# Performance work log

Hardware: AMD Instinct MI355X
Metric: run time of the kernel (lower is better)

## Reference

```python
import jax, jax.numpy as jnp
import numpy as np

EPS = 1e-08
TEMPERATURE = 0.05


def setup_inputs() -> dict:
    key = jax.random.key(0)
    k1, k2 = jax.random.split(key)
    N = 8192
    predict_similarity = jax.random.normal(k1, (N,), dtype=jnp.float32)
    true_similarity = jax.random.uniform(k2, (N,), dtype=jnp.float32)
    return {"predict_similarity": predict_similarity, "true_similarity": true_similarity}


def reference(predict_similarity, true_similarity):
    # Sort descending by ground-truth score
    order = jnp.argsort(-true_similarity)
    yt = true_similarity[order]                      # (N,)
    yp = (predict_similarity / TEMPERATURE)[order]   # (N,)
    N = yt.shape[0]

    # Pairwise ground-truth gaps W[k, j] = yt[k] - yt[j]
    W = yt[:, None] - yt[None, :]                    # (N, N)
    # negatives: strictly later in the sorted order AND strictly lower score
    tri = jnp.triu(jnp.ones((N, N), dtype=bool), 1)
    mask = tri & (W > EPS)
    row_valid = jnp.any(mask, axis=1)                # rows contributing to the loss

    neg_inf = jnp.float32(-jnp.inf)
    # weight for the positive = max gap among its valid negatives
    weight_k = jnp.max(jnp.where(mask, W, neg_inf), axis=1)
    weight_k = jnp.where(row_valid, weight_k, 0.0)

    logit_pos = yp * weight_k                        # (N,)
    L_neg = yp[None, :] * W                          # (N, N) negative logits

    # stable masked logsumexp over {pos} U {masked negatives}
    m = jnp.maximum(logit_pos, jnp.max(jnp.where(mask, L_neg, neg_inf), axis=1))
    m = jnp.where(row_valid, m, 0.0)
    z = jnp.where(mask, L_neg - m[:, None], neg_inf)  # exp(-inf)=0 for masked-out
    sum_exp = jnp.exp(logit_pos - m) + jnp.sum(jnp.exp(z), axis=1)
    log_prob = logit_pos - m - jnp.log(sum_exp)      # log_softmax(...)[0]

    count = jnp.sum(row_valid)
    total = jnp.sum(jnp.where(row_valid, log_prob, 0.0))
    return jnp.where(count > 0, -total / jnp.maximum(count, 1).astype(total.dtype), 0.0)
```

## Files before the change

kernel.cpp:

```cpp
#include <hip/hip_runtime.h>
#include <hip/hip_bf16.h>

#define NN 8192
#define EPSF 1e-8f
#define LOG2E 1.4426950408889634f
#define LN2f 0.6931471805599453f
#define BLOCK 256
#define ROWS 4
#define ROWS_PER_BLOCK (ROWS * (BLOCK / 64))
#define RG (NN / ROWS_PER_BLOCK)
#define CHUNKS 4
#define CH (NN / CHUNKS)

#define A2SCALE (20.0f * LOG2E)

__global__ __launch_bounds__(BLOCK) void pro_main(const float* __restrict__ yt_g,
                                                  const float* __restrict__ pred_g,
                                                  float2* __restrict__ partial) {
    __shared__ float4 yt_s[CH / 4];
    __shared__ float4 a2_s[CH / 4];

    const int t = threadIdx.x;
    const int rg = blockIdx.x >> 2;
    const int c  = blockIdx.x & 3;

    const float4* ytg4 = (const float4*)(yt_g + c * CH);
    const float4* pdg4 = (const float4*)(pred_g + c * CH);
    for (int i = t; i < CH / 4; i += BLOCK) {
        yt_s[i] = ytg4[i];
        float4 p = pdg4[i];
        p.x *= A2SCALE; p.y *= A2SCALE; p.z *= A2SCALE; p.w *= A2SCALE;
        a2_s[i] = p;
    }
    __syncthreads();

    const int wave = t >> 6, lane = t & 63;
    const int row0 = rg * ROWS_PER_BLOCK + wave * ROWS;

    float x[ROWS], M[ROWS];
#pragma unroll
    for (int r = 0; r < ROWS; ++r) {
        x[r] = yt_g[row0 + r];
        M[r] = -INFINITY;
    }

    for (int i = 0; i < CH / 256; ++i) {
        float4 y4 = yt_s[i * 64 + lane];
        float4 a4 = a2_s[i * 64 + lane];
#pragma unroll
        for (int r = 0; r < ROWS; ++r) {
            float W0 = x[r] - y4.x; float L0 = a4.x * W0; M[r] = fmaxf(M[r], (W0 > EPSF) ? L0 : -INFINITY);
            float W1 = x[r] - y4.y; float L1 = a4.y * W1; M[r] = fmaxf(M[r], (W1 > EPSF) ? L1 : -INFINITY);
            float W2 = x[r] - y4.z; float L2 = a4.z * W2; M[r] = fmaxf(M[r], (W2 > EPSF) ? L2 : -INFINITY);
            float W3 = x[r] - y4.w; float L3 = a4.w * W3; M[r] = fmaxf(M[r], (W3 > EPSF) ? L3 : -INFINITY);
        }
    }
#pragma unroll
    for (int r = 0; r < ROWS; ++r) {
#pragma unroll
        for (int m = 1; m < 64; m <<= 1) M[r] = fmaxf(M[r], __shfl_xor(M[r], m));
    }

    float s[ROWS] = {0.f, 0.f, 0.f, 0.f};
    for (int i = 0; i < CH / 256; ++i) {
        float4 y4 = yt_s[i * 64 + lane];
        float4 a4 = a2_s[i * 64 + lane];
#pragma unroll
        for (int r = 0; r < ROWS; ++r) {
            float W0 = x[r] - y4.x; float t0 = __builtin_fmaf(a4.x, W0, -M[r]); s[r] += exp2f((W0 > EPSF) ? t0 : -INFINITY);
            float W1 = x[r] - y4.y; float t1 = __builtin_fmaf(a4.y, W1, -M[r]); s[r] += exp2f((W1 > EPSF) ? t1 : -INFINITY);
            float W2 = x[r] - y4.z; float t2 = __builtin_fmaf(a4.z, W2, -M[r]); s[r] += exp2f((W2 > EPSF) ? t2 : -INFINITY);
            float W3 = x[r] - y4.w; float t3 = __builtin_fmaf(a4.w, W3, -M[r]); s[r] += exp2f((W3 > EPSF) ? t3 : -INFINITY);
        }
    }
#pragma unroll
    for (int r = 0; r < ROWS; ++r) {
#pragma unroll
        for (int m = 1; m < 64; m <<= 1) s[r] += __shfl_xor(s[r], m);
    }

    if (lane == 0) {
#pragma unroll
        for (int r = 0; r < ROWS; ++r) partial[c * NN + row0 + r] = make_float2(M[r], s[r]);
    }
}

__global__ __launch_bounds__(1024) void finalize(const float* __restrict__ yt,
                                                 const float* __restrict__ pred,
                                                 const float2* __restrict__ partial,
                                                 float* __restrict__ out) {
    __shared__ float redm[16];
    __shared__ float2 red2[16];
    __shared__ float bmin;
    const int t = threadIdx.x, lane = t & 63, wave = t >> 6;

    float mn = INFINITY;
    for (int i = t; i < NN; i += 1024) mn = fminf(mn, yt[i]);
#pragma unroll
    for (int m = 1; m < 64; m <<= 1) mn = fminf(mn, __shfl_xor(mn, m));
    if (lane == 0) redm[wave] = mn;
    __syncthreads();
    if (t == 0) {
        float v = redm[0];
        for (int i = 1; i < 16; ++i) v = fminf(v, redm[i]);
        bmin = v;
    }
    __syncthreads();
    const float yt_min = bmin;

    float wtot = 0.f, wcnt = 0.f;
    for (int row = t; row < NN; row += 1024) {
        float x = yt[row];
        float w = x - yt_min;
        float a2 = pred[row] * A2SCALE;
        float lp = a2 * w;
        float2 pc[CHUNKS];
        float M = lp;
#pragma unroll
        for (int c = 0; c < CHUNKS; ++c) {
            pc[c] = partial[c * NN + row];
            M = fmaxf(M, pc[c].x);
        }
        float sum = exp2f(lp - M);
#pragma unroll
        for (int c = 0; c < CHUNKS; ++c) sum += pc[c].y * exp2f(pc[c].x - M);
        float logp = (lp - M) * LN2f - __logf(sum);
        if (w > EPSF) { wtot += logp; wcnt += 1.f; }
    }
#pragma unroll
    for (int m = 1; m < 64; m <<= 1) { wtot += __shfl_xor(wtot, m); wcnt += __shfl_xor(wcnt, m); }
    if (lane == 0) red2[wave] = make_float2(wtot, wcnt);
    __syncthreads();
    if (t == 0) {
        float bt = 0.f, bc = 0.f;
        for (int i = 0; i < 16; ++i) { bt += red2[i].x; bc += red2[i].y; }
        out[0] = (bc > 0.f) ? (-bt / bc) : 0.f;
    }
}

extern "C" void kernel_launch(void* const* d_in, const int* in_sizes, int n_in,
                              void* d_out, int out_size, void* d_ws, size_t ws_size,
                              hipStream_t stream) {
    const float* pred = (const float*)d_in[0];
    const float* yt   = (const float*)d_in[1];

    float2* partial = (float2*)d_ws;

    pro_main<<<RG * CHUNKS, BLOCK, 0, stream>>>(yt, pred, partial);
    finalize<<<1, 1024, 0, stream>>>(yt, pred, partial, (float*)d_out);
}
```

Measured before the change: 93.02 us.

## Bucket-sort scores to skip non-negative column ranges in pairwise logsumexp

Adds a single-block counting sort that buckets ground-truth scores into 8192 bins and writes reordered scores and pre-scaled predictions plus bin offsets. The main kernel then processes rows in sorted order and stops at the row's bucket boundary, skipping columns that cannot be negatives. It also drops the mask test for columns in strictly lower buckets and precomputes a*y so each logit is one FMA. The cost is an extra launch with shared-memory atomics, and the bucket index assumes scores lie in [0,1); negative scores would index out of range.

Measured after the change: 98.83 us. +6.2%, slower.

```diff
diff --git a/kernel.cpp b/kernel.cpp
--- a/kernel.cpp
+++ b/kernel.cpp
@@ -2,91 +2,195 @@
 #include <hip/hip_bf16.h>
 
 #define NN 8192
+#define NB 8192
 #define EPSF 1e-8f
 #define LOG2E 1.4426950408889634f
 #define LN2f 0.6931471805599453f
 #define BLOCK 256
-#define ROWS 4
-#define ROWS_PER_BLOCK (ROWS * (BLOCK / 64))
-#define RG (NN / ROWS_PER_BLOCK)
 #define CHUNKS 4
 #define CH (NN / CHUNKS)
-
+#define RG (NN / 16)
 #define A2SCALE (20.0f * LOG2E)
 
-__global__ __launch_bounds__(BLOCK) void pro_main(const float* __restrict__ yt_g,
-                                                  const float* __restrict__ pred_g,
+__global__ __launch_bounds__(1024) void sort_kernel(const float* __restrict__ yt,
+                                                    const float* __restrict__ pred,
+                                                    float* __restrict__ ybkt,
+                                                    float* __restrict__ a2bkt,
+                                                    int* __restrict__ offs) {
+    __shared__ int hist[NB];
+    __shared__ int wsum[16], wexcl[16];
+    const int t = threadIdx.x, lane = t & 63, wave = t >> 6;
+
+    for (int k = t; k < NB; k += 1024) hist[k] = 0;
+    __syncthreads();
+
+    float yv[8]; int bv[8];
+#pragma unroll
+    for (int k = 0; k < 8; ++k) {
+        int i = t + k * 1024;
+        float y = yt[i];
+        int b = min((int)(y * 8192.0f), NB - 1);
+        yv[k] = y; bv[k] = b;
+        atomicAdd(&hist[b], 1);
+    }
+    __syncthreads();
+
+    int local[8]; int sum = 0;
+#pragma unroll
+    for (int k = 0; k < 8; ++k) { local[k] = hist[t * 8 + k]; sum += local[k]; }
+    int incl = sum;
+    for (int d = 1; d < 64; d <<= 1) {
+        int n = __shfl_up(incl, d);
+        if (lane >= d) incl += n;
+    }
+    if (lane == 63) wsum[wave] = incl;
+    __syncthreads();
+    if (t < 16) {
+        int v = wsum[t], inc2 = v;
+        for (int d = 1; d < 16; d <<= 1) {
+            int n = __shfl_up(inc2, d);
+            if (t >= d) inc2 += n;
+        }
+        wexcl[t] = inc2 - v;
+    }
+    __syncthreads();
+    int run = wexcl[wave] + incl - sum;
+#pragma unroll
+    for (int k = 0; k < 8; ++k) {
+        hist[t * 8 + k] = run;
+        offs[t * 8 + k] = run;
+        run += local[k];
+    }
+    if (t == 1023) offs[NB] = run;
+    __syncthreads();
+
+#pragma unroll
+    for (int k = 0; k < 8; ++k) {
+        int i = t + k * 1024;
+        int pos = atomicAdd(&hist[bv[k]], 1);
+        ybkt[pos] = yv[k];
+        a2bkt[pos] = pred[i] * A2SCALE;
+    }
+}
+
+__global__ __launch_bounds__(BLOCK) void pro_main(const float* __restrict__ ybkt,
+                                                  const float* __restrict__ a2bkt,
+                                                  const int* __restrict__ offs,
                                                   float2* __restrict__ partial) {
-    __shared__ float4 yt_s[CH / 4];
-    __shared__ float4 a2_s[CH / 4];
-
     const int t = threadIdx.x;
     const int rg = blockIdx.x >> 2;
     const int c  = blockIdx.x & 3;
-
-    const float4* ytg4 = (const float4*)(yt_g + c * CH);
-    const float4* pdg4 = (const float4*)(pred_g + c * CH);
-    for (int i = t; i < CH / 4; i += BLOCK) {
-        yt_s[i] = ytg4[i];
-        float4 p = pdg4[i];
-        p.x *= A2SCALE; p.y *= A2SCALE; p.z *= A2SCALE; p.w *= A2SCALE;
-        a2_s[i] = p;
-    }
-    __syncthreads();
-
+    const int j0 = c * CH;
     const int wave = t >> 6, lane = t & 63;
-    const int row0 = rg * ROWS_PER_BLOCK + wave * ROWS;
-
-    float x[ROWS], M[ROWS];
-#pragma unroll
-    for (int r = 0; r < ROWS; ++r) {
-        x[r] = yt_g[row0 + r];
-        M[r] = -INFINITY;
-    }
-
-    for (int i = 0; i < CH / 256; ++i) {
-        float4 y4 = yt_s[i * 64 + lane];
-        float4 a4 = a2_s[i * 64 + lane];
-#pragma unroll
-        for (int r = 0; r < ROWS; ++r) {
-            float W0 = x[r] - y4.x; float L0 = a4.x * W0; M[r] = fmaxf(M[r], (W0 > EPSF) ? L0 : -INFINITY);
-            float W1 = x[r] - y4.y; float L1 = a4.y * W1; M[r] = fmaxf(M[r], (W1 > EPSF) ? L1 : -INFINITY);
-            float W2 = x[r] - y4.z; float L2 = a4.z * W2; M[r] = fmaxf(M[r], (W2 > EPSF) ? L2 : -INFINITY);
-            float W3 = x[r] - y4.w; float L3 = a4.w * W3; M[r] = fmaxf(M[r], (W3 > EPSF) ? L3 : -INFINITY);
-        }
-    }
-#pragma unroll
-    for (int r = 0; r < ROWS; ++r) {
-#pragma unroll
+    const int row0 = rg * 16 + wave * 4;
+
+    {
+        float xl = ybkt[rg * 16 + 15];
+        int bl = min((int)(xl * 8192.0f), NB - 1);
+        if (offs[bl + 1] <= j0) {
+            if (lane == 0) {
+#pragma unroll
+                for (int r = 0; r < 4; ++r)
+                    partial[c * NN + row0 + r] = make_float2(-INFINITY, 0.0f);
+            }
+            return;
+        }
+    }
+
+    float x[4], M[4];
+#pragma unroll
+    for (int r = 0; r < 4; ++r) { x[r] = ybkt[row0 + r]; M[r] = -INFINITY; }
+    int u0, end3;
+    {
+        int b0 = min((int)(x[0] * 8192.0f), NB - 1);
+        u0 = (b0 > 0) ? offs[b0 - 1] : 0;
+        int b3 = min((int)(x[3] * 8192.0f), NB - 1);
+        end3 = offs[b3 + 1];
+    }
+    int lo = min(max(u0 - j0, 0), CH);
+    const int nbi = lo >> 7;
+    lo = nbi << 7;
+    const int hi = min(max(end3 - j0, lo), CH);
+    const int stage_n = min(CH, (hi + 127) & ~127);
+
+    __shared__ float y_s[CH];
+    __shared__ float4 ac_s[CH / 2];
+    const float4* yb4 = (const float4*)(ybkt + j0);
+    const float4* ab4 = (const float4*)(a2bkt + j0);
+    float4* ys4 = (float4*)y_s;
+    for (int i = t; i < stage_n / 4; i += BLOCK) {
+        float4 y4 = yb4[i];
+        float4 a4 = ab4[i];
+        ys4[i] = y4;
+        ac_s[2 * i]     = make_float4(a4.x, a4.x * y4.x, a4.y, a4.y * y4.y);
+        ac_s[2 * i + 1] = make_float4(a4.z, a4.z * y4.z, a4.w, a4.w * y4.w);
+    }
+    __syncthreads();
+
+    for (int i = 0; i < nbi; ++i) {
+        float4 v = ac_s[i * 64 + lane];
+#pragma unroll
+        for (int r = 0; r < 4; ++r) {
+            float L0 = __builtin_fmaf(v.x, x[r], -v.y);
+            float L1 = __builtin_fmaf(v.z, x[r], -v.w);
+            M[r] = fmaxf(M[r], fmaxf(L0, L1));
+        }
+    }
+    for (int base = lo; base < hi; base += 128) {
+        int e = base + lane * 2;
+        float y0 = y_s[e], y1 = y_s[e + 1];
+        float4 v = ac_s[(base >> 1) + lane];
+#pragma unroll
+        for (int r = 0; r < 4; ++r) {
+            float W0 = x[r] - y0, W1 = x[r] - y1;
+            float L0 = __builtin_fmaf(v.x, x[r], -v.y);
+            float L1 = __builtin_fmaf(v.z, x[r], -v.w);
+            L0 = (W0 > EPSF) ? L0 : -INFINITY;
+            L1 = (W1 > EPSF) ? L1 : -INFINITY;
+            M[r] = fmaxf(M[r], fmaxf(L0, L1));
+        }
+    }
+#pragma unroll
+    for (int r = 0; r < 4; ++r)
         for (int m = 1; m < 64; m <<= 1) M[r] = fmaxf(M[r], __shfl_xor(M[r], m));
-    }
-
-    float s[ROWS] = {0.f, 0.f, 0.f, 0.f};
-    for (int i = 0; i < CH / 256; ++i) {
-        float4 y4 = yt_s[i * 64 + lane];
-        float4 a4 = a2_s[i * 64 + lane];
-#pragma unroll
-        for (int r = 0; r < ROWS; ++r) {
-            float W0 = x[r] - y4.x; float t0 = __builtin_fmaf(a4.x, W0, -M[r]); s[r] += exp2f((W0 > EPSF) ? t0 : -INFINITY);
-            float W1 = x[r] - y4.y; float t1 = __builtin_fmaf(a4.y, W1, -M[r]); s[r] += exp2f((W1 > EPSF) ? t1 : -INFINITY);
-            float W2 = x[r] - y4.z; float t2 = __builtin_fmaf(a4.z, W2, -M[r]); s[r] += exp2f((W2 > EPSF) ? t2 : -INFINITY);
-            float W3 = x[r] - y4.w; float t3 = __builtin_fmaf(a4.w, W3, -M[r]); s[r] += exp2f((W3 > EPSF) ? t3 : -INFINITY);
-        }
-    }
-#pragma unroll
-    for (int r = 0; r < ROWS; ++r) {
-#pragma unroll
+
+    float s[4] = {0.f, 0.f, 0.f, 0.f};
+    for (int i = 0; i < nbi; ++i) {
+        float4 v = ac_s[i * 64 + lane];
+#pragma unroll
+        for (int r = 0; r < 4; ++r) {
+            float t0 = __builtin_fmaf(v.x, x[r], -v.y) - M[r];
+            float t1 = __builtin_fmaf(v.z, x[r], -v.w) - M[r];
+            s[r] += exp2f(t0) + exp2f(t1);
+        }
+    }
+    for (int base = lo; base < hi; base += 128) {
+        int e = base + lane * 2;
+        float y0 = y_s[e], y1 = y_s[e + 1];
+        float4 v = ac_s[(base >> 1) + lane];
+#pragma unroll
+        for (int r = 0; r < 4; ++r) {
+            float W0 = x[r] - y0, W1 = x[r] - y1;
+            float t0 = __builtin_fmaf(v.x, x[r], -v.y) - M[r];
+            float t1 = __builtin_fmaf(v.z, x[r], -v.w) - M[r];
+            t0 = (W0 > EPSF) ? t0 : -INFINITY;
+            t1 = (W1 > EPSF) ? t1 : -INFINITY;
+            s[r] += exp2f(t0) + exp2f(t1);
+        }
+    }
+#pragma unroll
+    for (int r = 0; r < 4; ++r)
         for (int m = 1; m < 64; m <<= 1) s[r] += __shfl_xor(s[r], m);
-    }
 
     if (lane == 0) {
 #pragma unroll
-        for (int r = 0; r < ROWS; ++r) partial[c * NN + row0 + r] = make_float2(M[r], s[r]);
-    }
-}
-
-__global__ __launch_bounds__(1024) void finalize(const float* __restrict__ yt,
-                                                 const float* __restrict__ pred,
+        for (int r = 0; r < 4; ++r)
+            partial[c * NN + row0 + r] = make_float2(M[r], s[r]);
+    }
+}
+
+__global__ __launch_bounds__(1024) void finalize(const float* __restrict__ ybkt,
+                                                 const float* __restrict__ a2bkt,
                                                  const float2* __restrict__ partial,
                                                  float* __restrict__ out) {
     __shared__ float redm[16];
@@ -95,7 +199,7 @@
     const int t = threadIdx.x, lane = t & 63, wave = t >> 6;
 
     float mn = INFINITY;
-    for (int i = t; i < NN; i += 1024) mn = fminf(mn, yt[i]);
+    for (int i = t; i < NN; i += 1024) mn = fminf(mn, ybkt[i]);
 #pragma unroll
     for (int m = 1; m < 64; m <<= 1) mn = fminf(mn, __shfl_xor(mn, m));
     if (lane == 0) redm[wave] = mn;
@@ -109,16 +213,15 @@
     const float yt_min = bmin;
 
     float wtot = 0.f, wcnt = 0.f;
-    for (int row = t; row < NN; row += 1024) {
-        float x = yt[row];
+    for (int p = t; p < NN; p += 1024) {
+        float x = ybkt[p];
         float w = x - yt_min;
-        float a2 = pred[row] * A2SCALE;
-        float lp = a2 * w;
+        float lp = a2bkt[p] * w;
         float2 pc[CHUNKS];
         float M = lp;
 #pragma unroll
         for (int c = 0; c < CHUNKS; ++c) {
-            pc[c] = partial[c * NN + row];
+            pc[c] = partial[c * NN + p];
             M = fmaxf(M, pc[c].x);
         }
         float sum = exp2f(lp - M);
@@ -144,8 +247,12 @@
     const float* pred = (const float*)d_in[0];
     const float* yt   = (const float*)d_in[1];
 
-    float2* partial = (float2*)d_ws;
-
-    pro_main<<<RG * CHUNKS, BLOCK, 0, stream>>>(yt, pred, partial);
-    finalize<<<1, 1024, 0, stream>>>(yt, pred, partial, (float*)d_out);
-}
+    float* ybkt  = (float*)d_ws;
+    float* a2bkt = ybkt + NN;
+    int*   offs  = (int*)(a2bkt + NN);
+    float2* partial = (float2*)(offs + NN + 2);
+
+    sort_kernel<<<1, 1024, 0, stream>>>(yt, pred, ybkt, a2bkt, offs);
+    pro_main<<<RG * CHUNKS, BLOCK, 0, stream>>>(ybkt, a2bkt, offs, partial);
+    finalize<<<1, 1024, 0, stream>>>(ybkt, a2bkt, partial, (float*)d_out);
+}
```

## Bucket-sort scores first to skip empty pair blocks and fuse finalize

Applied to the files above, without the earlier changes.

A new 32-block kernel bucket-sorts the true scores with a histogram, a prefix scan and a scatter, using hand-rolled grid barriers. The main kernel then works on the sorted data, so each row group only visits columns that can hold valid negatives: it skips whole chunks and drops the mask test on blocks fully below the row. This cuts the pairwise exp and max work roughly in half. The finalize step is folded into one block of the main kernel, which spins on per-block completion flags. The spin flags are never reset between launches, so repeated calls may race unless the workspace is cleared, and spinning blocks depend on every other block being scheduled.

Result: slower. 225.0 us (+141.9%).

```diff
diff --git a/kernel.cpp b/kernel.cpp
--- a/kernel.cpp
+++ b/kernel.cpp
@@ -2,139 +2,225 @@
 #include <hip/hip_bf16.h>
 
 #define NN 8192
+#define NB 8192
 #define EPSF 1e-8f
 #define LOG2E 1.4426950408889634f
 #define LN2f 0.6931471805599453f
-#define BLOCK 256
-#define ROWS 4
-#define ROWS_PER_BLOCK (ROWS * (BLOCK / 64))
-#define RG (NN / ROWS_PER_BLOCK)
 #define CHUNKS 4
 #define CH (NN / CHUNKS)
-
+#define KMAX (CH / 64)
+#define RG (NN / 16)
+#define NBLK (RG * CHUNKS)
 #define A2SCALE (20.0f * LOG2E)
 
-__global__ __launch_bounds__(BLOCK) void pro_main(const float* __restrict__ yt_g,
-                                                  const float* __restrict__ pred_g,
-                                                  float2* __restrict__ partial) {
-    __shared__ float4 yt_s[CH / 4];
-    __shared__ float4 a2_s[CH / 4];
-
-    const int t = threadIdx.x;
-    const int rg = blockIdx.x >> 2;
-    const int c  = blockIdx.x & 3;
-
-    const float4* ytg4 = (const float4*)(yt_g + c * CH);
-    const float4* pdg4 = (const float4*)(pred_g + c * CH);
-    for (int i = t; i < CH / 4; i += BLOCK) {
-        yt_s[i] = ytg4[i];
-        float4 p = pdg4[i];
-        p.x *= A2SCALE; p.y *= A2SCALE; p.z *= A2SCALE; p.w *= A2SCALE;
-        a2_s[i] = p;
-    }
-    __syncthreads();
-
-    const int wave = t >> 6, lane = t & 63;
-    const int row0 = rg * ROWS_PER_BLOCK + wave * ROWS;
-
-    float x[ROWS], M[ROWS];
-#pragma unroll
-    for (int r = 0; r < ROWS; ++r) {
-        x[r] = yt_g[row0 + r];
-        M[r] = -INFINITY;
-    }
-
-    for (int i = 0; i < CH / 256; ++i) {
-        float4 y4 = yt_s[i * 64 + lane];
-        float4 a4 = a2_s[i * 64 + lane];
-#pragma unroll
-        for (int r = 0; r < ROWS; ++r) {
-            float W0 = x[r] - y4.x; float L0 = a4.x * W0; M[r] = fmaxf(M[r], (W0 > EPSF) ? L0 : -INFINITY);
-            float W1 = x[r] - y4.y; float L1 = a4.y * W1; M[r] = fmaxf(M[r], (W1 > EPSF) ? L1 : -INFINITY);
-            float W2 = x[r] - y4.z; float L2 = a4.z * W2; M[r] = fmaxf(M[r], (W2 > EPSF) ? L2 : -INFINITY);
-            float W3 = x[r] - y4.w; float L3 = a4.w * W3; M[r] = fmaxf(M[r], (W3 > EPSF) ? L3 : -INFINITY);
-        }
-    }
-#pragma unroll
-    for (int r = 0; r < ROWS; ++r) {
-#pragma unroll
-        for (int m = 1; m < 64; m <<= 1) M[r] = fmaxf(M[r], __shfl_xor(M[r], m));
-    }
-
-    float s[ROWS] = {0.f, 0.f, 0.f, 0.f};
-    for (int i = 0; i < CH / 256; ++i) {
-        float4 y4 = yt_s[i * 64 + lane];
-        float4 a4 = a2_s[i * 64 + lane];
-#pragma unroll
-        for (int r = 0; r < ROWS; ++r) {
-            float W0 = x[r] - y4.x; float t0 = __builtin_fmaf(a4.x, W0, -M[r]); s[r] += exp2f((W0 > EPSF) ? t0 : -INFINITY);
-            float W1 = x[r] - y4.y; float t1 = __builtin_fmaf(a4.y, W1, -M[r]); s[r] += exp2f((W1 > EPSF) ? t1 : -INFINITY);
-            float W2 = x[r] - y4.z; float t2 = __builtin_fmaf(a4.z, W2, -M[r]); s[r] += exp2f((W2 > EPSF) ? t2 : -INFINITY);
-            float W3 = x[r] - y4.w; float t3 = __builtin_fmaf(a4.w, W3, -M[r]); s[r] += exp2f((W3 > EPSF) ? t3 : -INFINITY);
-        }
-    }
-#pragma unroll
-    for (int r = 0; r < ROWS; ++r) {
-#pragma unroll
-        for (int m = 1; m < 64; m <<= 1) s[r] += __shfl_xor(s[r], m);
-    }
-
-    if (lane == 0) {
-#pragma unroll
-        for (int r = 0; r < ROWS; ++r) partial[c * NN + row0 + r] = make_float2(M[r], s[r]);
-    }
-}
-
-__global__ __launch_bounds__(1024) void finalize(const float* __restrict__ yt,
-                                                 const float* __restrict__ pred,
-                                                 const float2* __restrict__ partial,
-                                                 float* __restrict__ out) {
-    __shared__ float redm[16];
-    __shared__ float2 red2[16];
-    __shared__ float bmin;
-    const int t = threadIdx.x, lane = t & 63, wave = t >> 6;
-
-    float mn = INFINITY;
-    for (int i = t; i < NN; i += 1024) mn = fminf(mn, yt[i]);
-#pragma unroll
-    for (int m = 1; m < 64; m <<= 1) mn = fminf(mn, __shfl_xor(mn, m));
-    if (lane == 0) redm[wave] = mn;
+__device__ __forceinline__ int bucket_of(float y) {
+    return min(max((int)(y * 8192.0f), 0), NB - 1);
+}
+
+__device__ __forceinline__ void barrier32(int* sflag, int b, int t, int gen) {
     __syncthreads();
     if (t == 0) {
-        float v = redm[0];
-        for (int i = 1; i < 16; ++i) v = fminf(v, redm[i]);
-        bmin = v;
+        __threadfence();
+        __hip_atomic_store(&sflag[b], gen, __ATOMIC_RELEASE, __HIP_MEMORY_SCOPE_AGENT);
+    }
+    if (t < 32) {
+        while (__hip_atomic_load(&sflag[t], __ATOMIC_ACQUIRE, __HIP_MEMORY_SCOPE_AGENT) < gen) {}
     }
     __syncthreads();
-    const float yt_min = bmin;
-
-    float wtot = 0.f, wcnt = 0.f;
-    for (int row = t; row < NN; row += 1024) {
-        float x = yt[row];
-        float w = x - yt_min;
-        float a2 = pred[row] * A2SCALE;
-        float lp = a2 * w;
-        float2 pc[CHUNKS];
-        float M = lp;
-#pragma unroll
-        for (int c = 0; c < CHUNKS; ++c) {
-            pc[c] = partial[c * NN + row];
-            M = fmaxf(M, pc[c].x);
-        }
-        float sum = exp2f(lp - M);
-#pragma unroll
-        for (int c = 0; c < CHUNKS; ++c) sum += pc[c].y * exp2f(pc[c].x - M);
-        float logp = (lp - M) * LN2f - __logf(sum);
-        if (w > EPSF) { wtot += logp; wcnt += 1.f; }
-    }
-#pragma unroll
-    for (int m = 1; m < 64; m <<= 1) { wtot += __shfl_xor(wtot, m); wcnt += __shfl_xor(wcnt, m); }
-    if (lane == 0) red2[wave] = make_float2(wtot, wcnt);
+}
+
+__global__ __launch_bounds__(256) void sort32(const float* __restrict__ yt,
+                                              const float* __restrict__ pred,
+                                              float* __restrict__ ybkt,
+                                              float* __restrict__ a2bkt,
+                                              int* __restrict__ offs,
+                                              int* __restrict__ hist,
+                                              int* __restrict__ cursor,
+                                              int* __restrict__ sflag) {
+    __shared__ int wred4[4];
+    const int t = threadIdx.x, b = blockIdx.x;
+    const int lane = t & 63, wave = t >> 6;
+    const int gid = b * 256 + t;
+
+    hist[gid] = 0;
+    barrier32(sflag, b, t, 1);
+
+    const float y = yt[gid];
+    const int bk = bucket_of(y);
+    atomicAdd(&hist[bk], 1);
+    barrier32(sflag, b, t, 2);
+
+    if (b == 0) {
+        const int base = t * 32;
+        int loc[32]; int sum = 0;
+#pragma unroll
+        for (int k = 0; k < 32; ++k) {
+            loc[k] = __hip_atomic_load(&hist[base + k], __ATOMIC_RELAXED, __HIP_MEMORY_SCOPE_AGENT);
+            sum += loc[k];
+        }
+        int incl = sum;
+        for (int d = 1; d < 64; d <<= 1) {
+            int n = __shfl_up(incl, d);
+            if (lane >= d) incl += n;
+        }
+        if (lane == 63) wred4[wave] = incl;
+        __syncthreads();
+        int wpre = 0;
+        for (int w2 = 0; w2 < 4; ++w2) wpre += (w2 < wave) ? wred4[w2] : 0;
+        int run = wpre + incl - sum;
+#pragma unroll
+        for (int k = 0; k < 32; ++k) {
+            offs[base + k] = run;
+            cursor[base + k] = run;
+            run += loc[k];
+        }
+        if (t == 255) offs[NB] = run;
+    }
+    barrier32(sflag, b, t, 3);
+
+    const int pos = atomicAdd(&cursor[bk], 1);
+    ybkt[pos] = y;
+    a2bkt[pos] = pred[gid] * A2SCALE;
+}
+
+__global__ __launch_bounds__(256, 4) void pro_fused(const float* __restrict__ ybkt,
+                                                    const float* __restrict__ a2bkt,
+                                                    const int* __restrict__ offs,
+                                                    float2* __restrict__ partial,
+                                                    int* __restrict__ pflag,
+                                                    float* __restrict__ out) {
+    __shared__ float fredm[4];
+    __shared__ float2 fred2[4];
+
+    const int t = threadIdx.x, lane = t & 63, wave = t >> 6;
+    const int braw = blockIdx.x;
+    const int rgl = braw >> 2, c = braw & 3;
+    const int rg = (rgl & 1) ? (RG - 1 - (rgl >> 1)) : (rgl >> 1);
+    const int j0 = c * CH;
+    const int row0 = rg * 16 + wave * 4;
+
+    const float x15 = ybkt[rg * 16 + 15];
+    const bool active = (offs[bucket_of(x15) + 1] > j0);
+
+    float M[4], s[4];
+#pragma unroll
+    for (int r = 0; r < 4; ++r) { M[r] = -INFINITY; s[r] = 0.0f; }
+
+    if (active) {
+        float x[4];
+#pragma unroll
+        for (int r = 0; r < 4; ++r) x[r] = ybkt[row0 + r];
+        const int b0 = bucket_of(x[0]), b3 = bucket_of(x[3]);
+        const int u0 = (b0 > 0) ? offs[b0 - 1] : 0;
+        const int e3 = offs[b3 + 1];
+        const int kfull = min(max((u0 - j0) >> 6, 0), KMAX);
+        const int kend  = min(max((e3 - j0 + 63) >> 6, kfull), KMAX);
+
+        float A[KMAX], C[KMAX];
+#pragma unroll
+        for (int k = 0; k < KMAX; ++k) {
+            if (k < kend) {
+                const int j = j0 + lane + (k << 6);
+                const float a = a2bkt[j];
+                A[k] = a;
+                C[k] = a * ybkt[j];
+            }
+        }
+
+#pragma unroll
+        for (int k = 0; k < KMAX; ++k) {
+            if (k < kfull) {
+#pragma unroll
+                for (int r = 0; r < 4; ++r)
+                    M[r] = fmaxf(M[r], __builtin_fmaf(A[k], x[r], -C[k]));
+            } else if (k < kend) {
+                const float yv = ybkt[j0 + lane + (k << 6)];
+#pragma unroll
+                for (int r = 0; r < 4; ++r) {
+                    const float W = x[r] - yv;
+                    const float L = __builtin_fmaf(A[k], x[r], -C[k]);
+                    M[r] = fmaxf(M[r], (W > EPSF) ? L : -INFINITY);
+                }
+            }
+        }
+#pragma unroll
+        for (int r = 0; r < 4; ++r)
+            for (int m = 1; m < 64; m <<= 1) M[r] = fmaxf(M[r], __shfl_xor(M[r], m));
+
+#pragma unroll
+        for (int k = 0; k < KMAX; ++k) {
+            if (k < kfull) {
+#pragma unroll
+                for (int r = 0; r < 4; ++r)
+                    s[r] += exp2f(__builtin_fmaf(A[k], x[r], -C[k]) - M[r]);
+            } else if (k < kend) {
+                const float yv = ybkt[j0 + lane + (k << 6)];
+#pragma unroll
+                for (int r = 0; r < 4; ++r) {
+                    const float W = x[r] - yv;
+                    const float tt = __builtin_fmaf(A[k], x[r], -C[k]) - M[r];
+                    s[r] += exp2f((W > EPSF) ? tt : -INFINITY);
+                }
+            }
+        }
+#pragma unroll
+        for (int r = 0; r < 4; ++r)
+            for (int m = 1; m < 64; m <<= 1) s[r] += __shfl_xor(s[r], m);
+    }
+
+    if (lane == 0) {
+#pragma unroll
+        for (int r = 0; r < 4; ++r)
+            partial[c * NN + row0 + r] = make_float2(M[r], s[r]);
+    }
+
     __syncthreads();
     if (t == 0) {
-        float bt = 0.f, bc = 0.f;
-        for (int i = 0; i < 16; ++i) { bt += red2[i].x; bc += red2[i].y; }
-        out[0] = (bc > 0.f) ? (-bt / bc) : 0.f;
+        __threadfence();
+        __hip_atomic_store(&pflag[braw], 1, __ATOMIC_RELEASE, __HIP_MEMORY_SCOPE_AGENT);
+    }
+
+    if (braw == 7) {
+        for (int i = t; i < NBLK; i += 256)
+            while (__hip_atomic_load(&pflag[i], __ATOMIC_ACQUIRE, __HIP_MEMORY_SCOPE_AGENT) < 1) {}
+        __syncthreads();
+        __threadfence();
+
+        float mn = INFINITY;
+        for (int i = t; i < NN; i += 256) mn = fminf(mn, ybkt[i]);
+#pragma unroll
+        for (int m = 1; m < 64; m <<= 1) mn = fminf(mn, __shfl_xor(mn, m));
+        if (lane == 0) fredm[wave] = mn;
+        __syncthreads();
+        const float ymin = fminf(fminf(fredm[0], fredm[1]), fminf(fredm[2], fredm[3]));
+
+        float wtot = 0.f, wcnt = 0.f;
+        for (int p = t; p < NN; p += 256) {
+            const float xv = ybkt[p];
+            const float w = xv - ymin;
+            const float lp = a2bkt[p] * w;
+            const float2 p0 = partial[0 * NN + p];
+            const float2 p1 = partial[1 * NN + p];
+            const float2 p2 = partial[2 * NN + p];
+            const float2 p3 = partial[3 * NN + p];
+            const float Mx = fmaxf(lp, fmaxf(fmaxf(p0.x, p1.x), fmaxf(p2.x, p3.x)));
+            float sum = exp2f(lp - Mx);
+            sum += p0.y * exp2f(p0.x - Mx);
+            sum += p1.y * exp2f(p1.x - Mx);
+            sum += p2.y * exp2f(p2.x - Mx);
+            sum += p3.y * exp2f(p3.x - Mx);
+            const float logp = (lp - Mx) * LN2f - __logf(sum);
+            if (w > EPSF) { wtot += logp; wcnt += 1.f; }
+        }
+#pragma unroll
+        for (int m = 1; m < 64; m <<= 1) { wtot += __shfl_xor(wtot, m); wcnt += __shfl_xor(wcnt, m); }
+        if (lane == 0) fred2[wave] = make_float2(wtot, wcnt);
+        __syncthreads();
+        if (t == 0) {
+            const float bt = fred2[0].x + fred2[1].x + fred2[2].x + fred2[3].x;
+            const float bc = fred2[0].y + fred2[1].y + fred2[2].y + fred2[3].y;
+            out[0] = (bc > 0.f) ? (-bt / bc) : 0.f;
+        }
     }
 }
 
@@ -144,8 +230,15 @@
     const float* pred = (const float*)d_in[0];
     const float* yt   = (const float*)d_in[1];
 
-    float2* partial = (float2*)d_ws;
-
-    pro_main<<<RG * CHUNKS, BLOCK, 0, stream>>>(yt, pred, partial);
-    finalize<<<1, 1024, 0, stream>>>(yt, pred, partial, (float*)d_out);
-}
+    float* ybkt   = (float*)d_ws;
+    float* a2bkt  = ybkt + NN;
+    int*   offs   = (int*)(a2bkt + NN);
+    int*   hist   = offs + NB + 8;
+    int*   cursor = hist + NB;
+    int*   sflag  = cursor + NB;
+    int*   pflag  = sflag + 64;
+    float2* partial = (float2*)(pflag + NBLK);
+
+    sort32<<<32, 256, 0, stream>>>(yt, pred, ybkt, a2bkt, offs, hist, cursor, sflag);
+    pro_fused<<<NBLK, 256, 0, stream>>>(ybkt, a2bkt, offs, partial, pflag, (float*)d_out);
+}
```
